# Kernel tuning notes

Hardware: AMD Instinct MI355X
Metric: run time of the kernel (lower is better)

Reference implementation:

```python
import jax, jax.numpy as jnp
import numpy as np

N_NODES = 20000
N_EDGES = 320000
IN_F = 256
OUT_F = 256
EDGE_F = 256


def _mlp2(x, W1, b1, W2, b2):
    # MLPLayers(2, [d_in, 2*d_in, d_out]) = Linear -> ReLU -> Linear
    return jax.nn.relu(x @ W1 + b1) @ W2 + b2


def setup_inputs() -> dict:
    key = jax.random.key(0)
    ks = jax.random.split(key, 12)

    def lin(k, fan_in, shape):
        bound = 1.0 / np.sqrt(fan_in)
        return jax.random.uniform(k, shape, jnp.float32, -bound, bound)

    node_feat = jax.random.normal(ks[0], (N_NODES, IN_F), jnp.float32)
    edge_feat = jax.random.normal(ks[1], (N_EDGES, EDGE_F), jnp.float32)
    src = jax.random.randint(ks[2], (N_EDGES,), 0, N_NODES, jnp.int32)
    dst = jax.random.randint(ks[3], (N_EDGES,), 0, N_NODES, jnp.int32)

    # edge_mlp: edge_feats -> 2*edge_feats -> in_feats
    We1 = lin(ks[4], EDGE_F, (EDGE_F, 2 * EDGE_F))
    be1 = lin(ks[5], EDGE_F, (2 * EDGE_F,))
    We2 = lin(ks[6], 2 * EDGE_F, (2 * EDGE_F, IN_F))
    be2 = lin(ks[7], 2 * EDGE_F, (IN_F,))
    # node mlp: in_feats -> 2*in_feats -> out_feats
    Wn1 = lin(ks[8], IN_F, (IN_F, 2 * IN_F))
    bn1 = lin(ks[9], IN_F, (2 * IN_F,))
    Wn2 = lin(ks[10], 2 * IN_F, (2 * IN_F, OUT_F))
    bn2 = lin(ks[11], 2 * IN_F, (OUT_F,))
    eps = jnp.zeros((1,), jnp.float32)

    return {"node_feat": node_feat, "edge_feat": edge_feat, "src": src, "dst": dst,
            "We1": We1, "be1": be1, "We2": We2, "be2": be2,
            "Wn1": Wn1, "bn1": bn1, "Wn2": Wn2, "bn2": bn2, "eps": eps}


def reference(node_feat, edge_feat, src, dst, We1, be1, We2, be2, Wn1, bn1, Wn2, bn2, eps):
    e = _mlp2(edge_feat, We1, be1, We2, be2)            # [E, IN_F]
    msg = jax.nn.relu(node_feat[src] + e)               # gather-add-relu
    out_h = jax.ops.segment_sum(msg, dst, num_segments=N_NODES)  # [N, IN_F]
    out = _mlp2((1.0 + eps[0]) * node_feat + out_h, Wn1, bn1, Wn2, bn2)
    return out
```

## Files before the change

kernel.cpp:

```cpp
#include <hip/hip_runtime.h>

#define NN  20000
#define NE  320000
#define FIN 256
#define FH  512

typedef __attribute__((ext_vector_type(8))) short bf16x8;
typedef __attribute__((ext_vector_type(4))) float f32x4;

static __device__ __forceinline__ unsigned short f2b(float f) {
    union { float f; unsigned int i; } v; v.f = f;
    return (unsigned short)((v.i + 0x7fffu + ((v.i >> 16) & 1u)) >> 16);
}
static __device__ __forceinline__ f32x4 mfma16(bf16x8 a, bf16x8 b, f32x4 c) {
    return __builtin_amdgcn_mfma_f32_16x16x32_bf16(a, b, c, 0, 0, 0);
}

__global__ void prep_weights(const float* __restrict__ We1, const float* __restrict__ We2,
                             const float* __restrict__ Wn1, const float* __restrict__ Wn2,
                             unsigned short* __restrict__ W1T, unsigned short* __restrict__ W2T,
                             unsigned short* __restrict__ Wn1T, unsigned short* __restrict__ Wn2T) {
    const int m = blockIdx.x >> 7;
    const int t = blockIdx.x & 127;
    const float* src; unsigned short* dst; int R, C;
    if      (m == 0) { src = We1; dst = W1T;  R = 256; C = 512; }
    else if (m == 1) { src = We2; dst = W2T;  R = 512; C = 256; }
    else if (m == 2) { src = Wn1; dst = Wn1T; R = 256; C = 512; }
    else             { src = Wn2; dst = Wn2T; R = 512; C = 256; }
    __shared__ unsigned short tl[32][33];
    const int tx  = threadIdx.x & 31;
    const int tyb = threadIdx.x >> 5;
    const int cb = C >> 5;
    const int bx = t % cb, by = t / cb;
    #pragma unroll
    for (int j = 0; j < 4; ++j)
        tl[tyb * 4 + j][tx] = f2b(src[(size_t)(by * 32 + tyb * 4 + j) * C + bx * 32 + tx]);
    __syncthreads();
    #pragma unroll
    for (int j = 0; j < 4; ++j)
        dst[(size_t)(bx * 32 + tyb * 4 + j) * R + by * 32 + tx] = tl[tx][tyb * 4 + j];
}

__global__ void hist_dst(const int* __restrict__ dstI, int* __restrict__ cnt) {
    int e = blockIdx.x * 256 + threadIdx.x;
    if (e < NE) atomicAdd(&cnt[dstI[e]], 1);
}

__global__ void scan_excl(const int* __restrict__ cnt, int* __restrict__ cursor) {
    __shared__ int s[1024];
    const int t = threadIdx.x;
    const int lo = t * 20;
    const int hi = (lo + 20 < NN) ? lo + 20 : NN;
    int sum = 0;
    for (int i = lo; i < hi; ++i) sum += cnt[i];
    s[t] = sum;
    __syncthreads();
    for (int off = 1; off < 1024; off <<= 1) {
        int v = (t >= off) ? s[t - off] : 0;
        __syncthreads();
        s[t] += v;
        __syncthreads();
    }
    int base = (t > 0) ? s[t - 1] : 0;
    for (int i = lo; i < hi; ++i) { cursor[i] = base; base += cnt[i]; }
}

__global__ void scatter_perm(const int* __restrict__ dstI,
                             int* __restrict__ cursor, int* __restrict__ perm) {
    int e = blockIdx.x * 256 + threadIdx.x;
    if (e < NE) {
        int pos = atomicAdd(&cursor[dstI[e]], 1);
        perm[pos] = e;
    }
}

__global__ void __launch_bounds__(256, 2)
gine_edge(const float* __restrict__ edge_feat,
          const float* __restrict__ node_feat,
          const int* __restrict__ srcI,
          const int* __restrict__ dstI,
          const int* __restrict__ perm,
          const unsigned short* __restrict__ W1T,
          const float* __restrict__ b1,
          const unsigned short* __restrict__ W2T,
          const float* __restrict__ b2,
          float* __restrict__ out_h)
{
    __shared__ union {
        unsigned short Xs[64 * 264];
        unsigned short Hs[64 * 512];
        float          Msg[64 * 260];
    } sh;
    __shared__ int snS[64], dnS[64], eS[64];

    const int tid  = threadIdx.x;
    const int wave = tid >> 6;
    const int lane = tid & 63;
    const int quad = lane >> 4;
    const int ln   = lane & 15;
    const int bs   = (blockIdx.x & 7) * 625 + (blockIdx.x >> 3);
    const int e0   = bs * 64;

    if (tid < 64) {
        const int e = perm[e0 + tid];
        eS[tid]  = e;
        snS[tid] = srcI[e];
        dnS[tid] = dstI[e];
    }
    __syncthreads();

    #pragma unroll
    for (int it = 0; it < 8; ++it) {
        const int chunk = tid + it * 256;
        const int row = chunk >> 5;
        const int c8  = (chunk & 31) << 3;
        const float* p = edge_feat + (size_t)eS[row] * FIN + c8;
        f32x4 o0 = *(const f32x4*)(p);
        f32x4 o1 = *(const f32x4*)(p + 4);
        bf16x8 pack;
        #pragma unroll
        for (int j = 0; j < 4; ++j) {
            pack[j]     = (short)f2b(o0[j]);
            pack[j + 4] = (short)f2b(o1[j]);
        }
        *(bf16x8*)(&sh.Xs[row * 264 + c8]) = pack;
    }
    __syncthreads();

    f32x4 zero4 = {0.f, 0.f, 0.f, 0.f};
    f32x4 acc1[4][8];
    #pragma unroll
    for (int rt = 0; rt < 4; ++rt)
        #pragma unroll
        for (int cw = 0; cw < 8; ++cw) acc1[rt][cw] = zero4;

    const unsigned short* bB = W1T + (wave * 128 + ln) * FIN + quad * 8;
    #pragma unroll
    for (int ks = 0; ks < 8; ++ks) {
        bf16x8 a[4], b[8];
        #pragma unroll
        for (int rt = 0; rt < 4; ++rt)
            a[rt] = *(const bf16x8*)(&sh.Xs[(rt * 16 + ln) * 264 + quad * 8 + ks * 32]);
        #pragma unroll
        for (int cw = 0; cw < 8; ++cw)
            b[cw] = *(const bf16x8*)(bB + cw * 16 * FIN + ks * 32);
        #pragma unroll
        for (int rt = 0; rt < 4; ++rt)
            #pragma unroll
            for (int cw = 0; cw < 8; ++cw)
                acc1[rt][cw] = mfma16(a[rt], b[cw], acc1[rt][cw]);
    }
    __syncthreads();

    #pragma unroll
    for (int cw = 0; cw < 8; ++cw) {
        const int n = wave * 128 + cw * 16 + ln;
        const float bias = b1[n];
        #pragma unroll
        for (int rt = 0; rt < 4; ++rt)
            #pragma unroll
            for (int r = 0; r < 4; ++r) {
                const int row = rt * 16 + quad * 4 + r;
                const float v = fmaxf(acc1[rt][cw][r] + bias, 0.f);
                sh.Hs[(row << 9) + (((n >> 3) ^ (row & 7)) << 3) + (n & 7)] = f2b(v);
            }
    }
    __syncthreads();

    f32x4 acc2[4][4];
    #pragma unroll
    for (int rt = 0; rt < 4; ++rt)
        #pragma unroll
        for (int cw = 0; cw < 4; ++cw) acc2[rt][cw] = zero4;

    #pragma unroll
    for (int ks = 0; ks < 16; ++ks) {
        const int kb = ks * 4 + quad;
        bf16x8 a[4], b[4];
        #pragma unroll
        for (int rt = 0; rt < 4; ++rt) {
            const int row = rt * 16 + ln;
            a[rt] = *(const bf16x8*)(&sh.Hs[(row << 9) + (((kb ^ (row & 7)) << 3))]);
        }
        #pragma unroll
        for (int cw = 0; cw < 4; ++cw)
            b[cw] = *(const bf16x8*)(W2T + (wave * 64 + cw * 16 + ln) * FH + kb * 8);
        #pragma unroll
        for (int rt = 0; rt < 4; ++rt)
            #pragma unroll
            for (int cw = 0; cw < 4; ++cw)
                acc2[rt][cw] = mfma16(a[rt], b[cw], acc2[rt][cw]);
    }
    __syncthreads();

    float biasv[4];
    #pragma unroll
    for (int cw = 0; cw < 4; ++cw)
        biasv[cw] = b2[wave * 64 + cw * 16 + ln];
    #pragma unroll
    for (int rt = 0; rt < 4; ++rt)
        #pragma unroll
        for (int r = 0; r < 4; ++r) {
            const int row = rt * 16 + quad * 4 + r;
            const int sn = snS[row];
            const float* nf = node_feat + (size_t)sn * FIN + wave * 64 + ln;
            #pragma unroll
            for (int cw = 0; cw < 4; ++cw) {
                const float e = acc2[rt][cw][r] + biasv[cw];
                sh.Msg[row * 260 + wave * 64 + cw * 16 + ln] =
                    fmaxf(nf[cw * 16] + e, 0.f);
            }
        }
    __syncthreads();

    {
        const int col = tid;
        const int d0 = dnS[0], d63 = dnS[63];
        float run = sh.Msg[col];
        int cur = d0;
        #pragma unroll 4
        for (int row = 1; row < 64; ++row) {
            const int d = dnS[row];
            if (d != cur) {
                if (cur == d0 || cur == d63)
                    atomicAdd(&out_h[(size_t)cur * FIN + col], run);
                else
                    out_h[(size_t)cur * FIN + col] = run;
                run = 0.f;
                cur = d;
            }
            run += sh.Msg[row * 260 + col];
        }
        atomicAdd(&out_h[(size_t)cur * FIN + col], run);
    }
}

__global__ void __launch_bounds__(256, 2)
gine_node(const float* __restrict__ node_feat,
          const float* __restrict__ out_h,
          const unsigned short* __restrict__ W1T,
          const float* __restrict__ b1,
          const unsigned short* __restrict__ W2T,
          const float* __restrict__ b2,
          const float* __restrict__ eps,
          float* __restrict__ out)
{
    __shared__ union {
        unsigned short Xs[64 * 264];
        unsigned short Hs[64 * 512];
    } sh;

    const int tid  = threadIdx.x;
    const int wave = tid >> 6;
    const int lane = tid & 63;
    const int quad = lane >> 4;
    const int ln   = lane & 15;
    const int n0   = blockIdx.x * 64;
    const float epsv = 1.0f + eps[0];

    #pragma unroll
    for (int it = 0; it < 8; ++it) {
        const int chunk = tid + it * 256;
        const int row = chunk >> 5;
        const int c8  = (chunk & 31) << 3;
        const int g   = n0 + row;
        bf16x8 pack = {0, 0, 0, 0, 0, 0, 0, 0};
        if (g < NN) {
            const float* pn = node_feat + (size_t)g * FIN + c8;
            const float* ph = out_h + (size_t)g * FIN + c8;
            f32x4 n0v = *(const f32x4*)(pn);
            f32x4 n1v = *(const f32x4*)(pn + 4);
            f32x4 h0v = *(const f32x4*)(ph);
            f32x4 h1v = *(const f32x4*)(ph + 4);
            #pragma unroll
            for (int j = 0; j < 4; ++j) {
                pack[j]     = (short)f2b(epsv * n0v[j] + h0v[j]);
                pack[j + 4] = (short)f2b(epsv * n1v[j] + h1v[j]);
            }
        }
        *(bf16x8*)(&sh.Xs[row * 264 + c8]) = pack;
    }
    __syncthreads();

    f32x4 zero4 = {0.f, 0.f, 0.f, 0.f};
    f32x4 acc1[4][8];
    #pragma unroll
    for (int rt = 0; rt < 4; ++rt)
        #pragma unroll
        for (int cw = 0; cw < 8; ++cw) acc1[rt][cw] = zero4;

    const unsigned short* bB = W1T + (wave * 128 + ln) * FIN + quad * 8;
    #pragma unroll
    for (int ks = 0; ks < 8; ++ks) {
        bf16x8 a[4], b[8];
        #pragma unroll
        for (int rt = 0; rt < 4; ++rt)
            a[rt] = *(const bf16x8*)(&sh.Xs[(rt * 16 + ln) * 264 + quad * 8 + ks * 32]);
        #pragma unroll
        for (int cw = 0; cw < 8; ++cw)
            b[cw] = *(const bf16x8*)(bB + cw * 16 * FIN + ks * 32);
        #pragma unroll
        for (int rt = 0; rt < 4; ++rt)
            #pragma unroll
            for (int cw = 0; cw < 8; ++cw)
                acc1[rt][cw] = mfma16(a[rt], b[cw], acc1[rt][cw]);
    }
    __syncthreads();

    #pragma unroll
    for (int cw = 0; cw < 8; ++cw) {
        const int n = wave * 128 + cw * 16 + ln;
        const float bias = b1[n];
        #pragma unroll
        for (int rt = 0; rt < 4; ++rt)
            #pragma unroll
            for (int r = 0; r < 4; ++r) {
                const int row = rt * 16 + quad * 4 + r;
                const float v = fmaxf(acc1[rt][cw][r] + bias, 0.f);
                sh.Hs[(row << 9) + (((n >> 3) ^ (row & 7)) << 3) + (n & 7)] = f2b(v);
            }
    }
    __syncthreads();

    f32x4 acc2[4][4];
    #pragma unroll
    for (int rt = 0; rt < 4; ++rt)
        #pragma unroll
        for (int cw = 0; cw < 4; ++cw) acc2[rt][cw] = zero4;

    #pragma unroll
    for (int ks = 0; ks < 16; ++ks) {
        const int kb = ks * 4 + quad;
        bf16x8 a[4], b[4];
        #pragma unroll
        for (int rt = 0; rt < 4; ++rt) {
            const int row = rt * 16 + ln;
            a[rt] = *(const bf16x8*)(&sh.Hs[(row << 9) + (((kb ^ (row & 7)) << 3))]);
        }
        #pragma unroll
        for (int cw = 0; cw < 4; ++cw)
            b[cw] = *(const bf16x8*)(W2T + (wave * 64 + cw * 16 + ln) * FH + kb * 8);
        #pragma unroll
        for (int rt = 0; rt < 4; ++rt)
            #pragma unroll
            for (int cw = 0; cw < 4; ++cw)
                acc2[rt][cw] = mfma16(a[rt], b[cw], acc2[rt][cw]);
    }

    float biasv[4];
    #pragma unroll
    for (int cw = 0; cw < 4; ++cw)
        biasv[cw] = b2[wave * 64 + cw * 16 + ln];
    #pragma unroll
    for (int rt = 0; rt < 4; ++rt)
        #pragma unroll
        for (int r = 0; r < 4; ++r) {
            const int row = rt * 16 + quad * 4 + r;
            const int g = n0 + row;
            if (g < NN) {
                #pragma unroll
                for (int cw = 0; cw < 4; ++cw)
                    out[(size_t)g * FIN + wave * 64 + cw * 16 + ln] =
                        acc2[rt][cw][r] + biasv[cw];
            }
        }
}

extern "C" void kernel_launch(void* const* d_in, const int* in_sizes, int n_in,
                              void* d_out, int out_size, void* d_ws, size_t ws_size,
                              hipStream_t stream) {
    const float* node_feat = (const float*)d_in[0];
    const float* edge_feat = (const float*)d_in[1];
    const int* srcI = (const int*)d_in[2];
    const int* dstI = (const int*)d_in[3];
    const float* We1 = (const float*)d_in[4];
    const float* be1 = (const float*)d_in[5];
    const float* We2 = (const float*)d_in[6];
    const float* be2 = (const float*)d_in[7];
    const float* Wn1 = (const float*)d_in[8];
    const float* bn1 = (const float*)d_in[9];
    const float* Wn2 = (const float*)d_in[10];
    const float* bn2 = (const float*)d_in[11];
    const float* eps = (const float*)d_in[12];

    char* ws = (char*)d_ws;
    float* out_h = (float*)ws;
    unsigned short* W1T  = (unsigned short*)(ws + 20480000);
    unsigned short* W2T  = W1T + 131072;
    unsigned short* Wn1T = W2T + 131072;
    unsigned short* Wn2T = Wn1T + 131072;
    int* cnt    = (int*)(ws + 20480000 + 4 * 262144);
    int* cursor = cnt + NN;
    int* perm   = cursor + NN;

    hipMemsetAsync(out_h, 0, (size_t)NN * FIN * sizeof(float), stream);
    hipMemsetAsync(cnt, 0, NN * sizeof(int), stream);

    prep_weights<<<512, 256, 0, stream>>>(We1, We2, Wn1, Wn2, W1T, W2T, Wn1T, Wn2T);

    hist_dst<<<(NE + 255) / 256, 256, 0, stream>>>(dstI, cnt);
    scan_excl<<<1, 1024, 0, stream>>>(cnt, cursor);
    scatter_perm<<<(NE + 255) / 256, 256, 0, stream>>>(dstI, cursor, perm);

    gine_edge<<<NE / 64, 256, 0, stream>>>(edge_feat, node_feat, srcI, dstI,
                                           perm, W1T, be1, W2T, be2, out_h);
    gine_node<<<(NN + 63) / 64, 256, 0, stream>>>(node_feat, out_h, Wn1T, bn1,
                                                  Wn2T, bn2, eps, (float*)d_out);
}
```

Before: 943.8 us.

## Swap MFMA operand roles to vectorize epilogues and cache counts in LDS scan

Both MLP kernels now pass the weight tile as the MFMA A operand and the edge/node tile as B, so each lane's accumulator holds four consecutive output features for one row. That lets bias loads, the bf16 hidden-layer store to LDS, the node_feat gather and the final output store use 4-wide vector accesses instead of scalar ones. The prefix-scan kernel also stages the whole count array in shared memory so the strided serial loops read LDS instead of global memory. Risks are a different LDS bank pattern for the u16x4 hidden writes and roughly 80KB of static shared memory in the scan kernel.

```diff
diff --git a/kernel.cpp b/kernel.cpp
--- a/kernel.cpp
+++ b/kernel.cpp
@@ -7,6 +7,7 @@
 
 typedef __attribute__((ext_vector_type(8))) short bf16x8;
 typedef __attribute__((ext_vector_type(4))) float f32x4;
+typedef __attribute__((ext_vector_type(4))) unsigned short u16x4;
 
 static __device__ __forceinline__ unsigned short f2b(float f) {
     union { float f; unsigned int i; } v; v.f = f;
@@ -14,6 +15,11 @@
 }
 static __device__ __forceinline__ f32x4 mfma16(bf16x8 a, bf16x8 b, f32x4 c) {
     return __builtin_amdgcn_mfma_f32_16x16x32_bf16(a, b, c, 0, 0, 0);
+}
+static __device__ __forceinline__ u16x4 pack4(float a, float b, float c, float d) {
+    u16x4 p;
+    p[0] = f2b(a); p[1] = f2b(b); p[2] = f2b(c); p[3] = f2b(d);
+    return p;
 }
 
 __global__ void prep_weights(const float* __restrict__ We1, const float* __restrict__ We2,
@@ -47,12 +53,15 @@
 }
 
 __global__ void scan_excl(const int* __restrict__ cnt, int* __restrict__ cursor) {
+    __shared__ int c[NN];
     __shared__ int s[1024];
     const int t = threadIdx.x;
+    for (int i = t; i < NN; i += 1024) c[i] = cnt[i];
+    __syncthreads();
     const int lo = t * 20;
     const int hi = (lo + 20 < NN) ? lo + 20 : NN;
     int sum = 0;
-    for (int i = lo; i < hi; ++i) sum += cnt[i];
+    for (int i = lo; i < hi; ++i) sum += c[i];
     s[t] = sum;
     __syncthreads();
     for (int off = 1; off < 1024; off <<= 1) {
@@ -62,7 +71,9 @@
         __syncthreads();
     }
     int base = (t > 0) ? s[t - 1] : 0;
-    for (int i = lo; i < hi; ++i) { cursor[i] = base; base += cnt[i]; }
+    for (int i = lo; i < hi; ++i) { int cv = c[i]; c[i] = base; base += cv; }
+    __syncthreads();
+    for (int i = t; i < NN; i += 1024) cursor[i] = c[i];
 }
 
 __global__ void scatter_perm(const int* __restrict__ dstI,
@@ -128,89 +139,89 @@
     __syncthreads();
 
     f32x4 zero4 = {0.f, 0.f, 0.f, 0.f};
-    f32x4 acc1[4][8];
-    #pragma unroll
-    for (int rt = 0; rt < 4; ++rt)
-        #pragma unroll
-        for (int cw = 0; cw < 8; ++cw) acc1[rt][cw] = zero4;
-
-    const unsigned short* bB = W1T + (wave * 128 + ln) * FIN + quad * 8;
+    f32x4 acc1[8][4];
+    #pragma unroll
+    for (int nt = 0; nt < 8; ++nt)
+        #pragma unroll
+        for (int et = 0; et < 4; ++et) acc1[nt][et] = zero4;
+
+    const unsigned short* wB = W1T + (wave * 128 + ln) * FIN + quad * 8;
     #pragma unroll
     for (int ks = 0; ks < 8; ++ks) {
-        bf16x8 a[4], b[8];
-        #pragma unroll
-        for (int rt = 0; rt < 4; ++rt)
-            a[rt] = *(const bf16x8*)(&sh.Xs[(rt * 16 + ln) * 264 + quad * 8 + ks * 32]);
-        #pragma unroll
-        for (int cw = 0; cw < 8; ++cw)
-            b[cw] = *(const bf16x8*)(bB + cw * 16 * FIN + ks * 32);
-        #pragma unroll
-        for (int rt = 0; rt < 4; ++rt)
-            #pragma unroll
-            for (int cw = 0; cw < 8; ++cw)
-                acc1[rt][cw] = mfma16(a[rt], b[cw], acc1[rt][cw]);
-    }
-    __syncthreads();
-
-    #pragma unroll
-    for (int cw = 0; cw < 8; ++cw) {
-        const int n = wave * 128 + cw * 16 + ln;
-        const float bias = b1[n];
-        #pragma unroll
-        for (int rt = 0; rt < 4; ++rt)
-            #pragma unroll
-            for (int r = 0; r < 4; ++r) {
-                const int row = rt * 16 + quad * 4 + r;
-                const float v = fmaxf(acc1[rt][cw][r] + bias, 0.f);
-                sh.Hs[(row << 9) + (((n >> 3) ^ (row & 7)) << 3) + (n & 7)] = f2b(v);
-            }
+        bf16x8 w[8], x[4];
+        #pragma unroll
+        for (int nt = 0; nt < 8; ++nt)
+            w[nt] = *(const bf16x8*)(wB + nt * 16 * FIN + ks * 32);
+        #pragma unroll
+        for (int et = 0; et < 4; ++et)
+            x[et] = *(const bf16x8*)(&sh.Xs[(et * 16 + ln) * 264 + quad * 8 + ks * 32]);
+        #pragma unroll
+        for (int nt = 0; nt < 8; ++nt)
+            #pragma unroll
+            for (int et = 0; et < 4; ++et)
+                acc1[nt][et] = mfma16(w[nt], x[et], acc1[nt][et]);
+    }
+    __syncthreads();
+
+    #pragma unroll
+    for (int nt = 0; nt < 8; ++nt) {
+        const int n0 = wave * 128 + nt * 16 + quad * 4;
+        const f32x4 b4 = *(const f32x4*)(b1 + n0);
+        #pragma unroll
+        for (int et = 0; et < 4; ++et) {
+            const int edge = et * 16 + ln;
+            u16x4 p = pack4(fmaxf(acc1[nt][et][0] + b4[0], 0.f),
+                            fmaxf(acc1[nt][et][1] + b4[1], 0.f),
+                            fmaxf(acc1[nt][et][2] + b4[2], 0.f),
+                            fmaxf(acc1[nt][et][3] + b4[3], 0.f));
+            *(u16x4*)(&sh.Hs[(edge << 9) + (((n0 >> 3) ^ (edge & 7)) << 3) + (n0 & 7)]) = p;
+        }
     }
     __syncthreads();
 
     f32x4 acc2[4][4];
     #pragma unroll
-    for (int rt = 0; rt < 4; ++rt)
-        #pragma unroll
-        for (int cw = 0; cw < 4; ++cw) acc2[rt][cw] = zero4;
-
+    for (int nt = 0; nt < 4; ++nt)
+        #pragma unroll
+        for (int et = 0; et < 4; ++et) acc2[nt][et] = zero4;
+
+    const unsigned short* w2B = W2T + (wave * 64 + ln) * FH;
     #pragma unroll
     for (int ks = 0; ks < 16; ++ks) {
         const int kb = ks * 4 + quad;
-        bf16x8 a[4], b[4];
-        #pragma unroll
-        for (int rt = 0; rt < 4; ++rt) {
-            const int row = rt * 16 + ln;
-            a[rt] = *(const bf16x8*)(&sh.Hs[(row << 9) + (((kb ^ (row & 7)) << 3))]);
-        }
-        #pragma unroll
-        for (int cw = 0; cw < 4; ++cw)
-            b[cw] = *(const bf16x8*)(W2T + (wave * 64 + cw * 16 + ln) * FH + kb * 8);
-        #pragma unroll
-        for (int rt = 0; rt < 4; ++rt)
-            #pragma unroll
-            for (int cw = 0; cw < 4; ++cw)
-                acc2[rt][cw] = mfma16(a[rt], b[cw], acc2[rt][cw]);
-    }
-    __syncthreads();
-
-    float biasv[4];
-    #pragma unroll
-    for (int cw = 0; cw < 4; ++cw)
-        biasv[cw] = b2[wave * 64 + cw * 16 + ln];
-    #pragma unroll
-    for (int rt = 0; rt < 4; ++rt)
-        #pragma unroll
-        for (int r = 0; r < 4; ++r) {
-            const int row = rt * 16 + quad * 4 + r;
-            const int sn = snS[row];
-            const float* nf = node_feat + (size_t)sn * FIN + wave * 64 + ln;
-            #pragma unroll
-            for (int cw = 0; cw < 4; ++cw) {
-                const float e = acc2[rt][cw][r] + biasv[cw];
-                sh.Msg[row * 260 + wave * 64 + cw * 16 + ln] =
-                    fmaxf(nf[cw * 16] + e, 0.f);
-            }
-        }
+        bf16x8 w[4], h[4];
+        #pragma unroll
+        for (int nt = 0; nt < 4; ++nt)
+            w[nt] = *(const bf16x8*)(w2B + nt * 16 * FH + kb * 8);
+        #pragma unroll
+        for (int et = 0; et < 4; ++et) {
+            const int edge = et * 16 + ln;
+            h[et] = *(const bf16x8*)(&sh.Hs[(edge << 9) + ((kb ^ (edge & 7)) << 3)]);
+        }
+        #pragma unroll
+        for (int nt = 0; nt < 4; ++nt)
+            #pragma unroll
+            for (int et = 0; et < 4; ++et)
+                acc2[nt][et] = mfma16(w[nt], h[et], acc2[nt][et]);
+    }
+    __syncthreads();
+
+    #pragma unroll
+    for (int nt = 0; nt < 4; ++nt) {
+        const int n0 = wave * 64 + nt * 16 + quad * 4;
+        const f32x4 b4 = *(const f32x4*)(b2 + n0);
+        #pragma unroll
+        for (int et = 0; et < 4; ++et) {
+            const int edge = et * 16 + ln;
+            const int sn = snS[edge];
+            const f32x4 nf = *(const f32x4*)(node_feat + (size_t)sn * FIN + n0);
+            f32x4 m;
+            #pragma unroll
+            for (int r = 0; r < 4; ++r)
+                m[r] = fmaxf(nf[r] + acc2[nt][et][r] + b4[r], 0.f);
+            *(f32x4*)(&sh.Msg[edge * 260 + n0]) = m;
+        }
+    }
     __syncthreads();
 
     {
@@ -255,7 +266,7 @@
     const int lane = tid & 63;
     const int quad = lane >> 4;
     const int ln   = lane & 15;
-    const int n0   = blockIdx.x * 64;
+    const int n0b  = blockIdx.x * 64;
     const float epsv = 1.0f + eps[0];
 
     #pragma unroll
@@ -263,7 +274,7 @@
         const int chunk = tid + it * 256;
         const int row = chunk >> 5;
         const int c8  = (chunk & 31) << 3;
-        const int g   = n0 + row;
+        const int g   = n0b + row;
         bf16x8 pack = {0, 0, 0, 0, 0, 0, 0, 0};
         if (g < NN) {
             const float* pn = node_feat + (size_t)g * FIN + c8;
@@ -283,87 +294,88 @@
     __syncthreads();
 
     f32x4 zero4 = {0.f, 0.f, 0.f, 0.f};
-    f32x4 acc1[4][8];
-    #pragma unroll
-    for (int rt = 0; rt < 4; ++rt)
-        #pragma unroll
-        for (int cw = 0; cw < 8; ++cw) acc1[rt][cw] = zero4;
-
-    const unsigned short* bB = W1T + (wave * 128 + ln) * FIN + quad * 8;
+    f32x4 acc1[8][4];
+    #pragma unroll
+    for (int nt = 0; nt < 8; ++nt)
+        #pragma unroll
+        for (int et = 0; et < 4; ++et) acc1[nt][et] = zero4;
+
+    const unsigned short* wB = W1T + (wave * 128 + ln) * FIN + quad * 8;
     #pragma unroll
     for (int ks = 0; ks < 8; ++ks) {
-        bf16x8 a[4], b[8];
-        #pragma unroll
-        for (int rt = 0; rt < 4; ++rt)
-            a[rt] = *(const bf16x8*)(&sh.Xs[(rt * 16 + ln) * 264 + quad * 8 + ks * 32]);
-        #pragma unroll
-        for (int cw = 0; cw < 8; ++cw)
-            b[cw] = *(const bf16x8*)(bB + cw * 16 * FIN + ks * 32);
-        #pragma unroll
-        for (int rt = 0; rt < 4; ++rt)
-            #pragma unroll
-            for (int cw = 0; cw < 8; ++cw)
-                acc1[rt][cw] = mfma16(a[rt], b[cw], acc1[rt][cw]);
-    }
-    __syncthreads();
-
-    #pragma unroll
-    for (int cw = 0; cw < 8; ++cw) {
-        const int n = wave * 128 + cw * 16 + ln;
-        const float bias = b1[n];
-        #pragma unroll
-        for (int rt = 0; rt < 4; ++rt)
-            #pragma unroll
-            for (int r = 0; r < 4; ++r) {
-                const int row = rt * 16 + quad * 4 + r;
-                const float v = fmaxf(acc1[rt][cw][r] + bias, 0.f);
-                sh.Hs[(row << 9) + (((n >> 3) ^ (row & 7)) << 3) + (n & 7)] = f2b(v);
-            }
+        bf16x8 w[8], x[4];
+        #pragma unroll
+        for (int nt = 0; nt < 8; ++nt)
+            w[nt] = *(const bf16x8*)(wB + nt * 16 * FIN + ks * 32);
+        #pragma unroll
+        for (int et = 0; et < 4; ++et)
+            x[et] = *(const bf16x8*)(&sh.Xs[(et * 16 + ln) * 264 + quad * 8 + ks * 32]);
+        #pragma unroll
+        for (int nt = 0; nt < 8; ++nt)
+            #pragma unroll
+            for (int et = 0; et < 4; ++et)
+                acc1[nt][et] = mfma16(w[nt], x[et], acc1[nt][et]);
+    }
+    __syncthreads();
+
+    #pragma unroll
+    for (int nt = 0; nt < 8; ++nt) {
+        const int n0 = wave * 128 + nt * 16 + quad * 4;
+        const f32x4 b4 = *(const f32x4*)(b1 + n0);
+        #pragma unroll
+        for (int et = 0; et < 4; ++et) {
+            const int edge = et * 16 + ln;
+            u16x4 p = pack4(fmaxf(acc1[nt][et][0] + b4[0], 0.f),
+                            fmaxf(acc1[nt][et][1] + b4[1], 0.f),
+                            fmaxf(acc1[nt][et][2] + b4[2], 0.f),
+                            fmaxf(acc1[nt][et][3] + b4[3], 0.f));
+            *(u16x4*)(&sh.Hs[(edge << 9) + (((n0 >> 3) ^ (edge & 7)) << 3) + (n0 & 7)]) = p;
+        }
     }
     __syncthreads();
 
     f32x4 acc2[4][4];
     #pragma unroll
-    for (int rt = 0; rt < 4; ++rt)
-        #pragma unroll
-        for (int cw = 0; cw < 4; ++cw) acc2[rt][cw] = zero4;
-
+    for (int nt = 0; nt < 4; ++nt)
+        #pragma unroll
+        for (int et = 0; et < 4; ++et) acc2[nt][et] = zero4;
+
+    const unsigned short* w2B = W2T + (wave * 64 + ln) * FH;
     #pragma unroll
     for (int ks = 0; ks < 16; ++ks) {
         const int kb = ks * 4 + quad;
-        bf16x8 a[4], b[4];
-        #pragma unroll
-        for (int rt = 0; rt < 4; ++rt) {
-            const int row = rt * 16 + ln;
-            a[rt] = *(const bf16x8*)(&sh.Hs[(row << 9) + (((kb ^ (row & 7)) << 3))]);
-        }
-        #pragma unroll
-        for (int cw = 0; cw < 4; ++cw)
-            b[cw] = *(const bf16x8*)(W2T + (wave * 64 + cw * 16 + ln) * FH + kb * 8);
-        #pragma unroll
-        for (int rt = 0; rt < 4; ++rt)
-            #pragma unroll
-            for (int cw = 0; cw < 4; ++cw)
-                acc2[rt][cw] = mfma16(a[rt], b[cw], acc2[rt][cw]);
-    }
-
-    float biasv[4];
-    #pragma unroll
-    for (int cw = 0; cw < 4; ++cw)
-        biasv[cw] = b2[wave * 64 + cw * 16 + ln];
-    #pragma unroll
-    for (int rt = 0; rt < 4; ++rt)
-        #pragma unroll
-        for (int r = 0; r < 4; ++r) {
-            const int row = rt * 16 + quad * 4 + r;
-            const int g = n0 + row;
+        bf16x8 w[4], h[4];
+        #pragma unroll
+        for (int nt = 0; nt < 4; ++nt)
+            w[nt] = *(const bf16x8*)(w2B + nt * 16 * FH + kb * 8);
+        #pragma unroll
+        for (int et = 0; et < 4; ++et) {
+            const int edge = et * 16 + ln;
+            h[et] = *(const bf16x8*)(&sh.Hs[(edge << 9) + ((kb ^ (edge & 7)) << 3)]);
+        }
+        #pragma unroll
+        for (int nt = 0; nt < 4; ++nt)
+            #pragma unroll
+            for (int et = 0; et < 4; ++et)
+                acc2[nt][et] = mfma16(w[nt], h[et], acc2[nt][et]);
+    }
+
+    #pragma unroll
+    for (int nt = 0; nt < 4; ++nt) {
+        const int n0 = wave * 64 + nt * 16 + quad * 4;
+        const f32x4 b4 = *(const f32x4*)(b2 + n0);
+        #pragma unroll
+        for (int et = 0; et < 4; ++et) {
+            const int g = n0b + et * 16 + ln;
             if (g < NN) {
+                f32x4 o;
                 #pragma unroll
-                for (int cw = 0; cw < 4; ++cw)
-                    out[(size_t)g * FIN + wave * 64 + cw * 16 + ln] =
-                        acc2[rt][cw][r] + biasv[cw];
+                for (int r = 0; r < 4; ++r)
+                    o[r] = acc2[nt][et][r] + b4[r];
+                *(f32x4*)(out + (size_t)g * FIN + n0) = o;
             }
         }
+    }
 }
 
 extern "C" void kernel_launch(void* const* d_in, const int* in_sizes, int n_in,
```

After: 947.1 us. Within noise of the previous version (+0.4%).
